# Performance work log

Measured on AMD Instinct MI355X. Metric: run time of the kernel, lower is better.

## Reference

```python
import jax, jax.numpy as jnp
import numpy as np

EPS = 1e-5  # torch LayerNorm default

def _ln(x, g, b):
    m = jnp.mean(x, axis=-1, keepdims=True)
    v = jnp.mean((x - m) ** 2, axis=-1, keepdims=True)
    return (x - m) / jnp.sqrt(v + EPS) * g + b

def _quantize_sym(t, n_bits):
    n_levels = 2 ** n_bits
    amax = jnp.maximum(jnp.max(jnp.abs(t)), 1e-8)
    scale = amax / (n_levels // 2 - 1)
    q = jnp.clip(jnp.round(t / scale), -(n_levels // 2), n_levels // 2 - 1)
    return q * scale

def setup_inputs() -> dict:
    key = jax.random.key(0)
    ks = jax.random.split(key, 8)
    L, D, H, dk, V, B, T = 2, 1024, 16, 64, 8192, 4, 2048
    inp = {}
    inp['input_ids'] = jax.random.randint(ks[0], (B, T), 0, V)
    inp['state_quant_bits'] = 16
    inp['embed_W'] = jax.random.normal(ks[1], (V, D), jnp.float32) * 0.02
    inp['conv_w'] = jax.random.normal(ks[2], (L, 3, 1, D), jnp.float32) * 0.3  # WIO depthwise layout
    inp['conv_b'] = jnp.zeros((L, D), jnp.float32)
    inp['Wqkv'] = jax.random.normal(ks[3], (L, 3 * D, D), jnp.float32) * 0.02
    inp['Wo'] = jax.random.normal(ks[4], (L, D, D), jnp.float32) * 0.02
    inp['W_LTM'] = jax.random.normal(ks[5], (L, H, dk, dk), jnp.float32) * 0.02
    inp['V_T0'] = jnp.zeros((L, H), jnp.float32)
    inp['V_gs'] = jnp.full((L, H), 0.5, jnp.float32)
    inp['beta_tau'] = jnp.ones((L, H), jnp.float32)
    inp['beta_gm'] = jnp.full((L, H), 0.1, jnp.float32)
    inp['C_ch'] = jnp.ones((L, H), jnp.float32)
    inp['gamma'] = jnp.full((L, H), 0.1, jnp.float32)
    inp['alpha_ppd'] = jnp.ones((L,), jnp.float32)
    inp['IC_threshold'] = jnp.full((L,), 0.5, jnp.float32)
    inp['ln1_g'] = jnp.ones((L, D), jnp.float32)
    inp['ln1_b'] = jnp.zeros((L, D), jnp.float32)
    inp['lnk_g'] = jnp.ones((L, dk), jnp.float32)
    inp['lnk_b'] = jnp.zeros((L, dk), jnp.float32)
    inp['ln_f_g'] = jnp.ones((D,), jnp.float32)
    inp['ln_f_b'] = jnp.zeros((D,), jnp.float32)
    inp['head_W'] = jax.random.normal(ks[6], (V, D), jnp.float32) * 0.02
    return inp

def _forward(input_ids, embed_W, conv_w, conv_b, Wqkv, Wo, W_LTM, V_T0, V_gs,
             beta_tau, beta_gm, C_ch, gamma, alpha_ppd, IC_threshold,
             ln1_g, ln1_b, lnk_g, lnk_b, ln_f_g, ln_f_b, head_W, state_quant_bits):
    B, T = input_ids.shape
    D = embed_W.shape[1]
    L, H = V_gs.shape
    dk = D // H
    x = embed_W[input_ids]  # (B,T,D)
    for l in range(L):
        residual = x
        h = _ln(x, ln1_g[l], ln1_b[l])
        # causal depthwise conv (torch pads 2 both sides then slices [:T] == left pad 2)
        hc = jax.lax.conv_general_dilated(
            h, conv_w[l], window_strides=(1,), padding=[(2, 0)],
            dimension_numbers=('NWC', 'WIO', 'NWC'), feature_group_count=D) + conv_b[l]
        h = h + hc
        qkv = h @ Wqkv[l].T  # (B,T,3D)
        q, k, v = jnp.split(qkv, 3, axis=-1)
        def heads(z):
            return z.reshape(B, T, H, dk).transpose(0, 2, 1, 3)  # (B,H,T,dk)
        q, k, v = heads(q), heads(k), heads(v)
        k = _ln(k, lnk_g[l], lnk_b[l])
        # static physics (H,dk,dk)
        V_eff = (V_gs[l] - V_T0[l])[:, None, None] + W_LTM[l]  # U_T = 1.0
        sp = jax.nn.softplus(V_eff)
        g_ch = beta_tau[l][:, None, None] * sp
        lam = 1.0 - jnp.exp(-g_ch / C_ch[l][:, None, None])
        G = beta_gm[l][:, None, None] * sp * jax.nn.sigmoid(V_eff)
        sign = jnp.tanh(alpha_ppd[l] * (g_ch - IC_threshold[l]))
        retention = 1.0 - lam
        gate = gamma[l][:, None, None] * sign * G
        Wl = W_LTM[l]
        qT = q.transpose(2, 0, 1, 3)  # (T,B,H,dk) time-major
        kT = k.transpose(2, 0, 1, 3)
        vT = v.transpose(2, 0, 1, 3)
        def step(F, qkv_t):
            qt, kt, vt = qkv_t  # (B,H,dk) each
            F = retention * F + gate * (vt[..., :, None] * kt[..., None, :])
            if state_quant_bits < 16:
                F = _quantize_sym(F, state_quant_bits)
            yt = jnp.einsum('bhvk,bhk->bhv', Wl + F, qt)
            return F, yt
        F0 = jnp.zeros((B, H, dk, dk), x.dtype)
        _, y = jax.lax.scan(step, F0, (qT, kT, vT))  # y: (T,B,H,dk)
        y = y.transpose(1, 0, 2, 3).reshape(B, T, D)
        x = residual + y @ Wo[l].T
    x = _ln(x, ln_f_g, ln_f_b)
    return x @ head_W.T  # (B,T,V)

def reference(input_ids, state_quant_bits, embed_W, conv_w, conv_b, Wqkv, Wo, W_LTM,
              V_T0, V_gs, beta_tau, beta_gm, C_ch, gamma, alpha_ppd, IC_threshold,
              ln1_g, ln1_b, lnk_g, lnk_b, ln_f_g, ln_f_b, head_W):
    return _forward(input_ids, embed_W, conv_w, conv_b, Wqkv, Wo, W_LTM, V_T0, V_gs,
                    beta_tau, beta_gm, C_ch, gamma, alpha_ppd, IC_threshold,
                    ln1_g, ln1_b, lnk_g, lnk_b, ln_f_g, ln_f_b, head_W, state_quant_bits)
```

## Files before the change

### kernel.cpp

```cpp
#include <hip/hip_runtime.h>

typedef unsigned short u16;
typedef __attribute__((ext_vector_type(8))) short bf16x8;
typedef __attribute__((ext_vector_type(4))) float f32x4;

__device__ __forceinline__ u16 f2b(float f) {
    union { unsigned int i; float f; } x; x.f = f;
    unsigned int r = (x.i + 0x7fffu + ((x.i >> 16) & 1u)) >> 16;
    return (u16)r;
}

__device__ __forceinline__ void gload16(const u16* g, u16* l) {
    __builtin_amdgcn_global_load_lds(
        (const __attribute__((address_space(1))) void*)g,
        (__attribute__((address_space(3))) void*)l, 16, 0, 0);
}

__global__ __launch_bounds__(256) void f2b_k(const float* __restrict__ in,
                                             u16* __restrict__ out, int n4) {
    const int i = blockIdx.x * 256 + threadIdx.x;
    if (i < n4) {
        float4 v = ((const float4*)in)[i];
        ushort4 o = { f2b(v.x), f2b(v.y), f2b(v.z), f2b(v.w) };
        ((ushort4*)out)[i] = o;
    }
}

__global__ __launch_bounds__(256) void embed_k(const int* __restrict__ ids,
                                               const float* __restrict__ E,
                                               float* __restrict__ x) {
    const int n = blockIdx.x, t = threadIdx.x;
    const int id = ids[n];
    float4 e = ((const float4*)(E + (size_t)id * 1024))[t];
    ((float4*)(x + (size_t)n * 1024))[t] = e;
}

__global__ __launch_bounds__(256) void physics_k(
        const float* __restrict__ W_LTM, const float* __restrict__ V_T0,
        const float* __restrict__ V_gs, const float* __restrict__ beta_tau,
        const float* __restrict__ beta_gm, const float* __restrict__ C_ch,
        const float* __restrict__ gammaP, const float* __restrict__ alphaP,
        const float* __restrict__ ICthr, float* __restrict__ ret,
        float* __restrict__ gat, float* __restrict__ rp) {
    const int idx = blockIdx.x * 256 + threadIdx.x;
    const int lh = idx >> 12;
    const int l  = lh >> 4;
    const float W    = W_LTM[idx];
    const float veff = V_gs[lh] - V_T0[lh] + W;
    const float sp   = fmaxf(veff, 0.f) + log1pf(expf(-fabsf(veff)));
    const float gch  = beta_tau[lh] * sp;
    const float G    = beta_gm[lh] * sp / (1.f + expf(-veff));
    const float sgn  = tanhf(alphaP[l] * (gch - ICthr[l]));
    const float e1   = gch / C_ch[lh];
    ret[idx] = expf(-e1);
    rp[idx]  = expf(-128.f * e1);
    gat[idx] = gammaP[lh] * sgn * G;
}

template<bool OUTB>
__global__ __launch_bounds__(256) void ln_rows(const float* __restrict__ X,
                                               const float* __restrict__ g,
                                               const float* __restrict__ bb,
                                               void* __restrict__ OUT) {
    const int n = blockIdx.x, t = threadIdx.x;
    const float4 xv = ((const float4*)(X + (size_t)n * 1024))[t];
    float s  = xv.x + xv.y + xv.z + xv.w;
    float s2 = xv.x * xv.x + xv.y * xv.y + xv.z * xv.z + xv.w * xv.w;
#pragma unroll
    for (int m = 32; m; m >>= 1) { s += __shfl_xor(s, m); s2 += __shfl_xor(s2, m); }
    __shared__ float sh[8];
    if ((t & 63) == 0) { sh[t >> 6] = s; sh[4 + (t >> 6)] = s2; }
    __syncthreads();
    s  = sh[0] + sh[1] + sh[2] + sh[3];
    s2 = sh[4] + sh[5] + sh[6] + sh[7];
    const float mean = s * (1.f / 1024.f);
    const float rstd = rsqrtf(s2 * (1.f / 1024.f) - mean * mean + 1e-5f);
    const int d0 = t * 4;
    const float4 gv = *(const float4*)&g[d0];
    const float4 bv = *(const float4*)&bb[d0];
    float o0 = (xv.x - mean) * rstd * gv.x + bv.x;
    float o1 = (xv.y - mean) * rstd * gv.y + bv.y;
    float o2 = (xv.z - mean) * rstd * gv.z + bv.z;
    float o3 = (xv.w - mean) * rstd * gv.w + bv.w;
    if (OUTB) {
        ushort4 o = { f2b(o0), f2b(o1), f2b(o2), f2b(o3) };
        ((ushort4*)((u16*)OUT + (size_t)n * 1024))[t] = o;
    } else {
        float4 o = { o0, o1, o2, o3 };
        ((float4*)((float*)OUT + (size_t)n * 1024))[t] = o;
    }
}

__global__ __launch_bounds__(256) void conv_k(const float* __restrict__ hln,
                                              const float* __restrict__ w,
                                              const float* __restrict__ cb,
                                              u16* __restrict__ out) {
    const int n = blockIdx.x;
    const int tt = n & 2047;
    const int d0 = threadIdx.x * 4;
    const float4 c = *(const float4*)&hln[(size_t)n * 1024 + d0];
    float4 m1 = { 0, 0, 0, 0 }, m2 = { 0, 0, 0, 0 };
    if (tt >= 1) m1 = *(const float4*)&hln[(size_t)(n - 1) * 1024 + d0];
    if (tt >= 2) m2 = *(const float4*)&hln[(size_t)(n - 2) * 1024 + d0];
    const float4 w0 = *(const float4*)&w[d0];
    const float4 w1 = *(const float4*)&w[1024 + d0];
    const float4 w2 = *(const float4*)&w[2048 + d0];
    const float4 cv = *(const float4*)&cb[d0];
    float o0 = c.x + m2.x * w0.x + m1.x * w1.x + c.x * w2.x + cv.x;
    float o1 = c.y + m2.y * w0.y + m1.y * w1.y + c.y * w2.y + cv.y;
    float o2 = c.z + m2.z * w0.z + m1.z * w1.z + c.z * w2.z + cv.z;
    float o3 = c.w + m2.w * w0.w + m1.w * w1.w + c.w * w2.w + cv.w;
    ushort4 o = { f2b(o0), f2b(o1), f2b(o2), f2b(o3) };
    *(ushort4*)&out[(size_t)n * 1024 + d0] = o;
}

__global__ __launch_bounds__(256) void kln_k(float* __restrict__ qkv,
                                             const float* __restrict__ g,
                                             const float* __restrict__ bb) {
    const int row = blockIdx.x * 4 + (threadIdx.x >> 6);
    const int lane = threadIdx.x & 63;
    const int n = row >> 4, h = row & 15;
    float* p = qkv + (size_t)n * 3072 + 1024 + h * 64 + lane;
    const float x = *p;
    float s = x, s2 = x * x;
#pragma unroll
    for (int m = 32; m; m >>= 1) { s += __shfl_xor(s, m); s2 += __shfl_xor(s2, m); }
    const float mean = s * (1.f / 64.f);
    const float rstd = rsqrtf(s2 * (1.f / 64.f) - mean * mean + 1e-5f);
    *p = (x - mean) * rstd * g[lane] + bb[lane];
}

template<int MODE>
__global__ __launch_bounds__(256, 2) void gemm_bt(const u16* __restrict__ A,
                                                  const u16* __restrict__ Bm,
                                                  float* __restrict__ C,
                                                  int Nn, int K) {
    __shared__ u16 lA[128 * 32];
    __shared__ u16 lB[128 * 32];
    const int t = threadIdx.x;
    const int lane = t & 63, wave = t >> 6;
    const int wm = (wave >> 1) * 64, wn = (wave & 1) * 64;
    const int m0 = blockIdx.y * 128, n0 = blockIdx.x * 128;
    f32x4 acc[4][4] = {};
    const int sr = t >> 2, sc = (t & 3) * 8;
    const u16* Ap = A + (size_t)(m0 + sr) * K + sc;
    const u16* Bp = Bm + (size_t)(n0 + sr) * K + sc;
    u16* lAw = lA + t * 8;
    u16* lBw = lB + t * 8;
    const int fr = lane & 15, fk = (lane >> 4) * 8;
    for (int k0 = 0; k0 < K; k0 += 32) {
        __syncthreads();
        gload16(Ap, lAw);
        gload16(Ap + (size_t)64 * K, lAw + 2048);
        gload16(Bp, lBw);
        gload16(Bp + (size_t)64 * K, lBw + 2048);
        Ap += 32; Bp += 32;
        __syncthreads();
        bf16x8 af[4], bf[4];
#pragma unroll
        for (int i = 0; i < 4; ++i) af[i] = *(const bf16x8*)&lA[(wm + i * 16 + fr) * 32 + fk];
#pragma unroll
        for (int i = 0; i < 4; ++i) bf[i] = *(const bf16x8*)&lB[(wn + i * 16 + fr) * 32 + fk];
#pragma unroll
        for (int i = 0; i < 4; ++i)
#pragma unroll
            for (int j = 0; j < 4; ++j)
                acc[i][j] = __builtin_amdgcn_mfma_f32_16x16x32_bf16(af[i], bf[j], acc[i][j], 0, 0, 0);
    }
    const int col = lane & 15, rw = (lane >> 4) * 4;
#pragma unroll
    for (int i = 0; i < 4; ++i)
#pragma unroll
        for (int j = 0; j < 4; ++j)
#pragma unroll
            for (int r = 0; r < 4; ++r) {
                const int gm = m0 + wm + i * 16 + rw + r;
                const int gn = n0 + wn + j * 16 + col;
                if (MODE == 0) C[(size_t)gm * Nn + gn] = acc[i][j][r];
                else           C[(size_t)gm * Nn + gn] += acc[i][j][r];
            }
}


__global__ __launch_bounds__(256, 4) void scanA_k(const float* __restrict__ qkv,
                                                  const float* __restrict__ ret,
                                                  const float* __restrict__ gat,
                                                  float* __restrict__ Floc) {
    const int bid = blockIdx.x;
    const int c = bid & 15, h = (bid >> 4) & 15, b = bid >> 8;
    const int i = threadIdx.x >> 2;
    const int j0 = (threadIdx.x & 3) * 16;
    const int base = (h * 64 + i) * 64 + j0;
    float r[16], g[16], F[16];
#pragma unroll
    for (int u = 0; u < 16; u += 4) {
        *(float4*)&r[u] = *(const float4*)&ret[base + u];
        *(float4*)&g[u] = *(const float4*)&gat[base + u];
    }
#pragma unroll
    for (int u = 0; u < 16; ++u) F[u] = 0.f;

    const size_t row0 = ((size_t)b * 2048 + (size_t)c * 128) * 3072;
    const float* bk = qkv + row0 + 1024 + h * 64 + j0;
    const float* bv = qkv + row0 + 2048 + h * 64 + i;

    float kA[16], kB[16], vA, vB;
#pragma unroll
    for (int u = 0; u < 16; u += 4) *(float4*)&kA[u] = *(const float4*)(bk + u);
    vA = *bv;

    unsigned offB = 3072, offA = 6144;
    for (int t = 0; t < 128; t += 2) {
#pragma unroll
        for (int u = 0; u < 16; u += 4) *(float4*)&kB[u] = *(const float4*)(bk + offB + u);
        vB = *(bv + offB);
        offB += 6144;
#pragma unroll
        for (int u = 0; u < 16; ++u) F[u] = r[u] * F[u] + (g[u] * kA[u]) * vA;
#pragma unroll
        for (int u = 0; u < 16; u += 4) *(float4*)&kA[u] = *(const float4*)(bk + offA + u);
        vA = *(bv + offA);
        offA += 6144;
#pragma unroll
        for (int u = 0; u < 16; ++u) F[u] = r[u] * F[u] + (g[u] * kB[u]) * vB;
    }
    float* Fo = Floc + ((size_t)((b * 16 + h) * 16 + c)) * 4096 + i * 64 + j0;
#pragma unroll
    for (int u = 0; u < 16; u += 4) *(float4*)&Fo[u] = *(const float4*)&F[u];
}

__global__ __launch_bounds__(256) void scanB_k(const float* __restrict__ rp,
                                               const float* __restrict__ Floc,
                                               float* __restrict__ Fin) {
    const int idx = blockIdx.x * 256 + threadIdx.x;
    const int e = idx & 4095;
    const int bh = idx >> 12;
    const int h = bh & 15;
    const float rpv = rp[h * 4096 + e];
    float F = 0.f;
#pragma unroll
    for (int c = 0; c < 16; ++c) {
        const size_t o = ((size_t)bh * 16 + c) * 4096 + e;
        Fin[o] = F;
        F = rpv * F + Floc[o];
    }
}

__global__ __launch_bounds__(256, 4) void scanC_k(const float* __restrict__ qkv,
                                                  const float* __restrict__ ret,
                                                  const float* __restrict__ gat,
                                                  const float* __restrict__ Wl,
                                                  const float* __restrict__ Fin,
                                                  u16* __restrict__ y) {
    const int bid = blockIdx.x;
    const int ig = bid & 1, c = (bid >> 1) & 15, h = (bid >> 5) & 15, b = bid >> 9;
    const int il = threadIdx.x >> 3;
    const int jq = threadIdx.x & 7;
    const int i = ig * 32 + il, j0 = jq * 8;
    const int base = (h * 64 + i) * 64 + j0;
    float r[8], g[8], w[8], F[8];
    const float* Fi = Fin + ((size_t)((b * 16 + h) * 16 + c)) * 4096 + i * 64 + j0;
#pragma unroll
    for (int u = 0; u < 8; u += 4) {
        *(float4*)&r[u] = *(const float4*)&ret[base + u];
        *(float4*)&g[u] = *(const float4*)&gat[base + u];
        *(float4*)&w[u] = *(const float4*)&Wl[base + u];
        *(float4*)&F[u] = *(const float4*)(Fi + u);
    }
    const size_t row0 = ((size_t)b * 2048 + (size_t)c * 128) * 3072;
    const float* bq = qkv + row0 + h * 64 + j0;
    const float* bk = bq + 1024;
    const float* bv = qkv + row0 + 2048 + h * 64 + i;
    u16* py = y + ((size_t)b * 2048 + (size_t)c * 128) * 1024 + h * 64 + i;

    float qA[8], qB[8], kA[8], kB[8], vA, vB;
#pragma unroll
    for (int u = 0; u < 8; u += 4) {
        *(float4*)&qA[u] = *(const float4*)(bq + u);
        *(float4*)&kA[u] = *(const float4*)(bk + u);
    }
    vA = *bv;

    unsigned offB = 3072, offA = 6144;
    for (int t = 0; t < 128; t += 2) {
#pragma unroll
        for (int u = 0; u < 8; u += 4) {
            *(float4*)&qB[u] = *(const float4*)(bq + offB + u);
            *(float4*)&kB[u] = *(const float4*)(bk + offB + u);
        }
        vB = *(bv + offB);
        offB += 6144;
        {
#pragma unroll
            for (int u = 0; u < 8; ++u) F[u] = r[u] * F[u] + (g[u] * kA[u]) * vA;
            float p0 = (w[0] + F[0]) * qA[0];
            float p1 = (w[1] + F[1]) * qA[1];
            p0 += (w[2] + F[2]) * qA[2];
            p1 += (w[3] + F[3]) * qA[3];
            p0 += (w[4] + F[4]) * qA[4];
            p1 += (w[5] + F[5]) * qA[5];
            p0 += (w[6] + F[6]) * qA[6];
            p1 += (w[7] + F[7]) * qA[7];
            float p = p0 + p1;
            p += __shfl_xor(p, 1);
            p += __shfl_xor(p, 2);
            p += __shfl_xor(p, 4);
            if (jq == 0) py[0] = f2b(p);
        }
#pragma unroll
        for (int u = 0; u < 8; u += 4) {
            *(float4*)&qA[u] = *(const float4*)(bq + offA + u);
            *(float4*)&kA[u] = *(const float4*)(bk + offA + u);
        }
        vA = *(bv + offA);
        offA += 6144;
        {
#pragma unroll
            for (int u = 0; u < 8; ++u) F[u] = r[u] * F[u] + (g[u] * kB[u]) * vB;
            float p0 = (w[0] + F[0]) * qB[0];
            float p1 = (w[1] + F[1]) * qB[1];
            p0 += (w[2] + F[2]) * qB[2];
            p1 += (w[3] + F[3]) * qB[3];
            p0 += (w[4] + F[4]) * qB[4];
            p1 += (w[5] + F[5]) * qB[5];
            p0 += (w[6] + F[6]) * qB[6];
            p1 += (w[7] + F[7]) * qB[7];
            float p = p0 + p1;
            p += __shfl_xor(p, 1);
            p += __shfl_xor(p, 2);
            p += __shfl_xor(p, 4);
            if (jq == 0) py[1024] = f2b(p);
        }
        py += 2048;
    }
}

extern "C" void kernel_launch(void* const* d_in, const int* in_sizes, int n_in,
                              void* d_out, int out_size, void* d_ws, size_t ws_size,
                              hipStream_t stream) {
    constexpr int Bz = 4, T = 2048, Dd = 1024, Hh = 16, Vv = 8192, Ll = 2;
    constexpr int Nn = Bz * T;
    const int*   ids      = (const int*)d_in[0];
    const float* embed_W  = (const float*)d_in[2];
    const float* conv_w   = (const float*)d_in[3];
    const float* conv_b   = (const float*)d_in[4];
    const float* Wqkv     = (const float*)d_in[5];
    const float* Wo       = (const float*)d_in[6];
    const float* W_LTM    = (const float*)d_in[7];
    const float* V_T0     = (const float*)d_in[8];
    const float* V_gs     = (const float*)d_in[9];
    const float* beta_tau = (const float*)d_in[10];
    const float* beta_gm  = (const float*)d_in[11];
    const float* C_ch     = (const float*)d_in[12];
    const float* gammaP   = (const float*)d_in[13];
    const float* alphaP   = (const float*)d_in[14];
    const float* ICthr    = (const float*)d_in[15];
    const float* ln1_g    = (const float*)d_in[16];
    const float* ln1_b    = (const float*)d_in[17];
    const float* lnk_g    = (const float*)d_in[18];
    const float* lnk_b    = (const float*)d_in[19];
    const float* lnf_g    = (const float*)d_in[20];
    const float* lnf_b    = (const float*)d_in[21];
    const float* head_W   = (const float*)d_in[22];

    float* x    = (float*)d_ws;
    float* qkvF = x + (size_t)Nn * Dd;
    float* ret  = qkvF + (size_t)Nn * 3 * Dd;
    float* gat  = ret + (size_t)Ll * Hh * 4096;
    float* rp   = gat + (size_t)Ll * Hh * 4096;
    float* hln  = rp + (size_t)Ll * Hh * 4096;
    u16*  yb    = (u16*)hln;
    u16*  xf    = yb + (size_t)Nn * Dd;
    float* Fin  = (float*)xf;
    u16*  hb    = (u16*)(hln + (size_t)Nn * Dd);
    float* Floc = (float*)hb;
    u16*  wq_b  = hb + (size_t)Nn * Dd;
    u16*  wo_b  = wq_b + (size_t)Ll * 3 * Dd * Dd;
    u16*  wh_b  = wo_b + (size_t)Ll * Dd * Dd;

    f2b_k<<<(Ll * 3 * Dd * Dd / 4 + 255) / 256, 256, 0, stream>>>(Wqkv, wq_b, Ll * 3 * Dd * Dd / 4);
    f2b_k<<<(Ll * Dd * Dd / 4 + 255) / 256, 256, 0, stream>>>(Wo, wo_b, Ll * Dd * Dd / 4);
    f2b_k<<<(Vv * Dd / 4 + 255) / 256, 256, 0, stream>>>(head_W, wh_b, Vv * Dd / 4);

    embed_k<<<Nn, 256, 0, stream>>>(ids, embed_W, x);
    physics_k<<<(Ll * Hh * 4096) / 256, 256, 0, stream>>>(W_LTM, V_T0, V_gs, beta_tau,
                                                          beta_gm, C_ch, gammaP, alphaP,
                                                          ICthr, ret, gat, rp);
    for (int l = 0; l < Ll; ++l) {
        const float* retl = ret + (size_t)l * Hh * 4096;
        const float* gatl = gat + (size_t)l * Hh * 4096;
        ln_rows<false><<<Nn, 256, 0, stream>>>(x, ln1_g + l * Dd, ln1_b + l * Dd, hln);
        conv_k<<<Nn, 256, 0, stream>>>(hln, conv_w + l * 3 * Dd, conv_b + l * Dd, hb);
        gemm_bt<0><<<dim3(3 * Dd / 128, Nn / 128), 256, 0, stream>>>(
            hb, wq_b + (size_t)l * 3 * Dd * Dd, qkvF, 3 * Dd, Dd);
        kln_k<<<Nn * Hh / 4, 256, 0, stream>>>(qkvF, lnk_g + l * 64, lnk_b + l * 64);
        scanA_k<<<Bz * Hh * 16, 256, 0, stream>>>(qkvF, retl, gatl, Floc);
        scanB_k<<<Bz * Hh * 4096 / 256, 256, 0, stream>>>(rp + (size_t)l * Hh * 4096, Floc, Fin);
        scanC_k<<<Bz * Hh * 16 * 2, 256, 0, stream>>>(qkvF, retl, gatl,
                                                      W_LTM + (size_t)l * Hh * 4096, Fin, yb);
        gemm_bt<1><<<dim3(Dd / 128, Nn / 128), 256, 0, stream>>>(
            yb, wo_b + (size_t)l * Dd * Dd, x, Dd, Dd);
    }
    ln_rows<true><<<Nn, 256, 0, stream>>>(x, lnf_g, lnf_b, xf);
    gemm_bt<0><<<dim3(Vv / 128, Nn / 128), 256, 0, stream>>>(xf, wh_b, (float*)d_out, Vv, Dd);
}
```

Before: 1.420 ms.

## Add 256x256-tile pipelined bf16 GEMM for QKV and head projections

Adds a new 512-thread GEMM kernel that computes 256x256 output tiles. It double-buffers K-slices of 64 in LDS using direct global-to-LDS loads with an XOR swizzle, and interleaves half-tile MFMA bursts with prefetch of the next slice, raising wave priority during MFMAs. Blocks are remapped across 8 groups, which looks aimed at spreading tiles over the XCDs. The kernel replaces the 128x128 GEMM for the QKV projection and the large vocabulary head GEMM, to raise data reuse and MFMA utilisation. In exchange it uses 128 KB of LDS per block and many accumulator registers, which limits occupancy, and for the QKV GEMM it launches fewer blocks.

```diff
diff --git a/kernel.cpp b/kernel.cpp
--- a/kernel.cpp
+++ b/kernel.cpp
@@ -181,6 +181,141 @@
             }
 }
 
+template<int MODE>
+__global__ __launch_bounds__(512, 2) void gemm256(const u16* __restrict__ A,
+                                                  const u16* __restrict__ Bm,
+                                                  float* __restrict__ C,
+                                                  int Nn, int K, int ntiles) {
+    __shared__ u16 lds[65536];
+    const int tid = threadIdx.x;
+    const int lane = tid & 63, wave = tid >> 6;
+    const int wm = wave >> 2, wn = wave & 3;
+    const int nwg = gridDim.x;
+    const int cpx = nwg >> 3;
+    const int bid0 = blockIdx.x;
+    const int bid = (bid0 & 7) * cpx + (bid0 >> 3);
+    const int m0 = (bid / ntiles) * 256, n0 = (bid % ntiles) * 256;
+
+    const int sr = tid >> 2;
+    const int sc = (tid & 3) ^ ((tid >> 3) & 3);
+    const u16* gA = A + (size_t)(m0 + sr) * K + sc * 8;
+    const u16* gB = Bm + (size_t)(n0 + sr) * K + sc * 8;
+    const size_t qstep = (size_t)128 * K;
+    const int ldst = tid * 8;
+
+    const int laneRow = lane & 15, g4 = lane >> 4;
+    const int swz = g4 ^ ((laneRow >> 1) & 3);
+    const int pA = ((wm * 128 + laneRow) * 4 + swz) * 8;
+    const int pB = ((wn * 64 + laneRow) * 4 + swz) * 8;
+
+    f32x4 acc[8][4] = {};
+    const int NT = K >> 6;
+
+    {
+        u16* d = (u16*)lds;
+        gload16(gA,              d + ldst);
+        gload16(gA + qstep,      d + 4096 + ldst);
+        gload16(gB,              d + 16384 + ldst);
+        gload16(gB + qstep,      d + 16384 + 4096 + ldst);
+        gload16(gA + 32,         d + 8192 + ldst);
+        gload16(gA + 32 + qstep, d + 8192 + 4096 + ldst);
+        gload16(gB + 32,         d + 24576 + ldst);
+        gload16(gB + 32 + qstep, d + 24576 + 4096 + ldst);
+    }
+    asm volatile("s_waitcnt vmcnt(4)" ::: "memory");
+    __builtin_amdgcn_s_barrier();
+
+    for (int t = 0; t < NT; ++t) {
+        const u16* lb = lds + (t & 1) * 32768;
+        u16* sb = (u16*)lds + ((t + 1) & 1) * 32768;
+        const bool st = (t + 1 < NT);
+        const int ko = (t + 1) * 64;
+        bf16x8 a[8], b0, b1, b2, b3;
+
+#pragma unroll
+        for (int f = 0; f < 8; ++f) a[f] = *(const bf16x8*)(lb + pA + f * 512);
+        b0 = *(const bf16x8*)(lb + 16384 + pB);
+        b1 = *(const bf16x8*)(lb + 16384 + pB + 512);
+        if (st) { gload16(gA + ko, sb + ldst); gload16(gA + ko + qstep, sb + 4096 + ldst); }
+        __builtin_amdgcn_s_barrier();
+        asm volatile("s_waitcnt lgkmcnt(0)" ::: "memory");
+        __builtin_amdgcn_sched_barrier(0);
+        __builtin_amdgcn_s_setprio(1);
+#pragma unroll
+        for (int m = 0; m < 8; ++m) {
+            acc[m][0] = __builtin_amdgcn_mfma_f32_16x16x32_bf16(a[m], b0, acc[m][0], 0, 0, 0);
+            acc[m][1] = __builtin_amdgcn_mfma_f32_16x16x32_bf16(a[m], b1, acc[m][1], 0, 0, 0);
+        }
+        __builtin_amdgcn_s_setprio(0);
+        __builtin_amdgcn_s_barrier();
+
+        b2 = *(const bf16x8*)(lb + 16384 + pB + 1024);
+        b3 = *(const bf16x8*)(lb + 16384 + pB + 1536);
+        if (st) { gload16(gB + ko, sb + 16384 + ldst); gload16(gB + ko + qstep, sb + 16384 + 4096 + ldst); }
+        if (st) asm volatile("s_waitcnt vmcnt(4)" ::: "memory");
+        else    asm volatile("s_waitcnt vmcnt(0)" ::: "memory");
+        __builtin_amdgcn_s_barrier();
+        asm volatile("s_waitcnt lgkmcnt(0)" ::: "memory");
+        __builtin_amdgcn_sched_barrier(0);
+        __builtin_amdgcn_s_setprio(1);
+#pragma unroll
+        for (int m = 0; m < 8; ++m) {
+            acc[m][2] = __builtin_amdgcn_mfma_f32_16x16x32_bf16(a[m], b2, acc[m][2], 0, 0, 0);
+            acc[m][3] = __builtin_amdgcn_mfma_f32_16x16x32_bf16(a[m], b3, acc[m][3], 0, 0, 0);
+        }
+        __builtin_amdgcn_s_setprio(0);
+        __builtin_amdgcn_s_barrier();
+
+#pragma unroll
+        for (int f = 0; f < 8; ++f) a[f] = *(const bf16x8*)(lb + 8192 + pA + f * 512);
+        b0 = *(const bf16x8*)(lb + 24576 + pB);
+        b1 = *(const bf16x8*)(lb + 24576 + pB + 512);
+        if (st) { gload16(gA + ko + 32, sb + 8192 + ldst); gload16(gA + ko + 32 + qstep, sb + 8192 + 4096 + ldst); }
+        __builtin_amdgcn_s_barrier();
+        asm volatile("s_waitcnt lgkmcnt(0)" ::: "memory");
+        __builtin_amdgcn_sched_barrier(0);
+        __builtin_amdgcn_s_setprio(1);
+#pragma unroll
+        for (int m = 0; m < 8; ++m) {
+            acc[m][0] = __builtin_amdgcn_mfma_f32_16x16x32_bf16(a[m], b0, acc[m][0], 0, 0, 0);
+            acc[m][1] = __builtin_amdgcn_mfma_f32_16x16x32_bf16(a[m], b1, acc[m][1], 0, 0, 0);
+        }
+        __builtin_amdgcn_s_setprio(0);
+        __builtin_amdgcn_s_barrier();
+
+        b2 = *(const bf16x8*)(lb + 24576 + pB + 1024);
+        b3 = *(const bf16x8*)(lb + 24576 + pB + 1536);
+        if (st) { gload16(gB + ko + 32, sb + 24576 + ldst); gload16(gB + ko + 32 + qstep, sb + 24576 + 4096 + ldst); }
+        if (st) asm volatile("s_waitcnt vmcnt(4)" ::: "memory");
+        else    asm volatile("s_waitcnt vmcnt(0)" ::: "memory");
+        __builtin_amdgcn_s_barrier();
+        asm volatile("s_waitcnt lgkmcnt(0)" ::: "memory");
+        __builtin_amdgcn_sched_barrier(0);
+        __builtin_amdgcn_s_setprio(1);
+#pragma unroll
+        for (int m = 0; m < 8; ++m) {
+            acc[m][2] = __builtin_amdgcn_mfma_f32_16x16x32_bf16(a[m], b2, acc[m][2], 0, 0, 0);
+            acc[m][3] = __builtin_amdgcn_mfma_f32_16x16x32_bf16(a[m], b3, acc[m][3], 0, 0, 0);
+        }
+        __builtin_amdgcn_s_setprio(0);
+        __builtin_amdgcn_s_barrier();
+    }
+
+    const int col = lane & 15, rw4 = (lane >> 4) * 4;
+    const int gm0 = m0 + wm * 128, gn0 = n0 + wn * 64;
+#pragma unroll
+    for (int m = 0; m < 8; ++m)
+#pragma unroll
+        for (int n = 0; n < 4; ++n) {
+            float* cp = C + (size_t)(gm0 + m * 16 + rw4) * Nn + gn0 + n * 16 + col;
+#pragma unroll
+            for (int r = 0; r < 4; ++r) {
+                if (MODE == 0) cp[(size_t)r * Nn] = acc[m][n][r];
+                else           cp[(size_t)r * Nn] += acc[m][n][r];
+            }
+        }
+}
+
 
 __global__ __launch_bounds__(256, 4) void scanA_k(const float* __restrict__ qkv,
                                                   const float* __restrict__ ret,
@@ -391,8 +526,8 @@
         const float* gatl = gat + (size_t)l * Hh * 4096;
         ln_rows<false><<<Nn, 256, 0, stream>>>(x, ln1_g + l * Dd, ln1_b + l * Dd, hln);
         conv_k<<<Nn, 256, 0, stream>>>(hln, conv_w + l * 3 * Dd, conv_b + l * Dd, hb);
-        gemm_bt<0><<<dim3(3 * Dd / 128, Nn / 128), 256, 0, stream>>>(
-            hb, wq_b + (size_t)l * 3 * Dd * Dd, qkvF, 3 * Dd, Dd);
+        gemm256<0><<<(Nn / 256) * (3 * Dd / 256), 512, 0, stream>>>(
+            hb, wq_b + (size_t)l * 3 * Dd * Dd, qkvF, 3 * Dd, Dd, 3 * Dd / 256);
         kln_k<<<Nn * Hh / 4, 256, 0, stream>>>(qkvF, lnk_g + l * 64, lnk_b + l * 64);
         scanA_k<<<Bz * Hh * 16, 256, 0, stream>>>(qkvF, retl, gatl, Floc);
         scanB_k<<<Bz * Hh * 4096 / 256, 256, 0, stream>>>(rp + (size_t)l * Hh * 4096, Floc, Fin);
@@ -402,5 +537,6 @@
             yb, wo_b + (size_t)l * Dd * Dd, x, Dd, Dd);
     }
     ln_rows<true><<<Nn, 256, 0, stream>>>(x, lnf_g, lnf_b, xf);
-    gemm_bt<0><<<dim3(Vv / 128, Nn / 128), 256, 0, stream>>>(xf, wh_b, (float*)d_out, Vv, Dd);
-}
+    gemm256<0><<<(Nn / 256) * (Vv / 256), 512, 0, stream>>>(
+        xf, wh_b, (float*)d_out, Vv, Dd, Vv / 256);
+}
```

After: 1.418 ms. Within noise of the previous version (-0.1%).
